# Kernel optimization log

Hardware: AMD Instinct MI355X
Metric: run time of the kernel (lower is better)

Reference implementation:

```python
import jax, jax.numpy as jnp
import numpy as np


def _binarize_except_outliers(weight):
    # torch.mean / torch.std over the flattened weight; torch.std is unbiased (ddof=1)
    mean = jnp.mean(weight)
    std = jnp.std(weight, ddof=1)
    lower = mean - std
    upper = mean + std
    outliers = (weight < lower) | (weight > upper)
    # non-outliers -> sign(w) (STEBinary forward); outliers keep original fp values
    return jnp.where(outliers, weight, jnp.sign(weight))


def setup_inputs() -> dict:
    key = jax.random.key(0)
    k1, k2, k3 = jax.random.split(key, 3)
    B, S, D_IN, D_OUT = 8, 2048, 4096, 4096
    x = jax.random.normal(k1, (B, S, D_IN), dtype=jnp.float32)
    weight = jax.random.normal(k2, (D_OUT, D_IN), dtype=jnp.float32) * 0.02
    bias = jax.random.normal(k3, (D_OUT,), dtype=jnp.float32) * 0.02
    return {"x": x, "weight": weight, "bias": bias}


def reference(x, weight, bias):
    w_bin = _binarize_except_outliers(weight)  # [d_out, d_in]
    # F.linear: x @ w.T + b
    out = jnp.einsum("bsd,od->bso", x, w_bin) + bias
    return out
```

## Files before the change

### kernel.cpp

```cpp
#include <hip/hip_runtime.h>
#include <stdint.h>
#include <math.h>

typedef __attribute__((ext_vector_type(8))) short short8;
typedef __attribute__((ext_vector_type(4))) float f32x4;

typedef const __attribute__((address_space(1))) void* gas_ptr;
typedef __attribute__((address_space(3))) void* las_ptr;

__device__ __forceinline__ void gld_lds16(const void* g, void* l) {
    __builtin_amdgcn_global_load_lds((gas_ptr)g, (las_ptr)l, 16, 0, 0);
}

__device__ __forceinline__ unsigned short f32_to_bf16_rne(float f) {
    unsigned u = __builtin_bit_cast(unsigned, f);
    u += 0x7FFFu + ((u >> 16) & 1u);
    return (unsigned short)(u >> 16);
}

__global__ void stats_partial_kernel(const float* __restrict__ w, int n4, double* __restrict__ partials) {
    __shared__ double ssum[256];
    __shared__ double ssq[256];
    int t = threadIdx.x;
    long i = (long)blockIdx.x * blockDim.x + t;
    long stride = (long)gridDim.x * blockDim.x;
    double s = 0.0, q = 0.0;
    for (; i < n4; i += stride) {
        float4 v = ((const float4*)w)[i];
        s += (double)v.x + (double)v.y + (double)v.z + (double)v.w;
        q += (double)v.x * v.x + (double)v.y * v.y + (double)v.z * v.z + (double)v.w * v.w;
    }
    ssum[t] = s; ssq[t] = q;
    __syncthreads();
    for (int off = 128; off > 0; off >>= 1) {
        if (t < off) { ssum[t] += ssum[t + off]; ssq[t] += ssq[t + off]; }
        __syncthreads();
    }
    if (t == 0) {
        partials[2 * blockIdx.x]     = ssum[0];
        partials[2 * blockIdx.x + 1] = ssq[0];
    }
}

__global__ void stats_final_kernel(const double* __restrict__ partials, int nblocks, long n,
                                   float* __restrict__ bounds) {
    __shared__ double ssum[256];
    __shared__ double ssq[256];
    int t = threadIdx.x;
    double s = 0.0, q = 0.0;
    for (int i = t; i < nblocks; i += 256) {
        s += partials[2 * i];
        q += partials[2 * i + 1];
    }
    ssum[t] = s; ssq[t] = q;
    __syncthreads();
    for (int off = 128; off > 0; off >>= 1) {
        if (t < off) { ssum[t] += ssum[t + off]; ssq[t] += ssq[t + off]; }
        __syncthreads();
    }
    if (t == 0) {
        double sum = ssum[0], sumsq = ssq[0];
        double mean = sum / (double)n;
        double var = (sumsq - sum * sum / (double)n) / (double)(n - 1);
        double sd = sqrt(var);
        bounds[0] = (float)(mean - sd);
        bounds[1] = (float)(mean + sd);
    }
}

__global__ void binarize_w_kernel(const float* __restrict__ w, const float* __restrict__ bounds,
                                  unsigned short* __restrict__ wb, long n4) {
    float lo = bounds[0], hi = bounds[1];
    long i = (long)blockIdx.x * blockDim.x + threadIdx.x;
    if (i >= n4) return;
    float4 v = ((const float4*)w)[i];
    float r[4] = {v.x, v.y, v.z, v.w};
    ushort4 o;
    unsigned short ob[4];
#pragma unroll
    for (int j = 0; j < 4; j++) {
        float f = r[j];
        bool outlier = (f < lo) || (f > hi);
        float b = outlier ? f : (f > 0.f ? 1.f : (f < 0.f ? -1.f : 0.f));
        ob[j] = f32_to_bf16_rne(b);
    }
    o.x = ob[0]; o.y = ob[1]; o.z = ob[2]; o.w = ob[3];
    ((ushort4*)wb)[i] = o;
}

__global__ void convert_x_kernel(const float* __restrict__ x, unsigned short* __restrict__ xb, long n4) {
    long i = (long)blockIdx.x * blockDim.x + threadIdx.x;
    if (i >= n4) return;
    float4 v = ((const float4*)x)[i];
    ushort4 o;
    o.x = f32_to_bf16_rne(v.x);
    o.y = f32_to_bf16_rne(v.y);
    o.z = f32_to_bf16_rne(v.z);
    o.w = f32_to_bf16_rne(v.w);
    ((ushort4*)xb)[i] = o;
}

#define BM 128
#define BN 128
#define BK 64

__global__ __launch_bounds__(256) void gemm_bt_kernel(
    const unsigned short* __restrict__ A,
    const unsigned short* __restrict__ B,
    const float* __restrict__ bias,
    float* __restrict__ C,
    int M, int N, int K)
{
    __shared__ __align__(16) unsigned short As[BM * BK];
    __shared__ __align__(16) unsigned short Bs[BN * BK];

    const int t = threadIdx.x;
    const int wave = t >> 6;
    const int lane = t & 63;
    const int wr = wave >> 1;
    const int wc = wave & 1;
    const int lm = lane & 15;
    const int quad = lane >> 4;
    const int sw = lm & 7;

    const int tile_m = blockIdx.y * BM;
    const int tile_n = blockIdx.x * BN;

    f32x4 acc[4][4] = {};

    int row_[4], src_[4];
#pragma unroll
    for (int j = 0; j < 4; j++) {
        int c = j * 256 + t;
        int r = c >> 3, kc = c & 7;
        row_[j] = r;
        src_[j] = (kc ^ (r & 7)) * 8;
    }
    const int lds_base = wave * 512;

    const size_t Astripe = (size_t)tile_m * K;
    const size_t Bstripe = (size_t)tile_n * K;

    for (int kt = 0; kt < K; kt += BK) {
#pragma unroll
        for (int j = 0; j < 4; j++) {
            gld_lds16(A + Astripe + (size_t)row_[j] * K + kt + src_[j], &As[j * 2048 + lds_base]);
            gld_lds16(B + Bstripe + (size_t)row_[j] * K + kt + src_[j], &Bs[j * 2048 + lds_base]);
        }
        __syncthreads();

#pragma unroll
        for (int s = 0; s < 2; s++) {
            short8 af[4], bf[4];
#pragma unroll
            for (int i = 0; i < 4; i++) {
                int arow = wr * 64 + i * 16 + lm;
                int achunk = (s * 4 + quad) ^ sw;
                af[i] = *(const short8*)&As[arow * 64 + achunk * 8];
                int brow = wc * 64 + i * 16 + lm;
                bf[i] = *(const short8*)&Bs[brow * 64 + achunk * 8];
            }
#pragma unroll
            for (int i = 0; i < 4; i++)
#pragma unroll
                for (int j = 0; j < 4; j++)
                    acc[i][j] = __builtin_amdgcn_mfma_f32_16x16x32_bf16(af[i], bf[j], acc[i][j], 0, 0, 0);
        }
        __syncthreads();
    }

#pragma unroll
    for (int j = 0; j < 4; j++) {
        int col = tile_n + wc * 64 + j * 16 + lm;
        float bv = bias[col];
#pragma unroll
        for (int i = 0; i < 4; i++) {
            int row0 = tile_m + wr * 64 + i * 16 + quad * 4;
#pragma unroll
            for (int r = 0; r < 4; r++) {
                C[(size_t)(row0 + r) * N + col] = acc[i][j][r] + bv;
            }
        }
    }
}

__global__ void gemm_fallback_kernel(const float* __restrict__ A, const float* __restrict__ W,
                                     const float* __restrict__ bias, const float* __restrict__ bounds,
                                     float* __restrict__ C, int M, int N, int K) {
    __shared__ float as[16][16];
    __shared__ float wsm[16][17];
    int tx = threadIdx.x, ty = threadIdx.y;
    int row = blockIdx.y * 16 + ty;
    int col = blockIdx.x * 16 + tx;
    float lo = bounds[0], hi = bounds[1];
    float acc = 0.f;
    for (int k0 = 0; k0 < K; k0 += 16) {
        as[ty][tx] = A[(size_t)row * K + k0 + tx];
        float wv = W[(size_t)(blockIdx.x * 16 + ty) * K + k0 + tx];
        bool outlier = (wv < lo) || (wv > hi);
        wsm[ty][tx] = outlier ? wv : (wv > 0.f ? 1.f : (wv < 0.f ? -1.f : 0.f));
        __syncthreads();
#pragma unroll
        for (int k = 0; k < 16; k++) acc += as[ty][k] * wsm[tx][k];
        __syncthreads();
    }
    C[(size_t)row * N + col] = acc + bias[col];
}

extern "C" void kernel_launch(void* const* d_in, const int* in_sizes, int n_in,
                              void* d_out, int out_size, void* d_ws, size_t ws_size,
                              hipStream_t stream) {
    const float* x    = (const float*)d_in[0];
    const float* w    = (const float*)d_in[1];
    const float* bias = (const float*)d_in[2];
    float* out = (float*)d_out;

    const int  N  = in_sizes[2];
    const long wn = (long)in_sizes[1];
    const int  K  = (int)(wn / N);
    const long xn = (long)in_sizes[0];
    const int  M  = (int)(xn / K);

    char* ws = (char*)d_ws;
    float*  bounds   = (float*)ws;
    double* partials = (double*)(ws + 64);
    const size_t wb_off = 16512;
    unsigned short* wb = (unsigned short*)(ws + wb_off);
    const size_t xb_off = wb_off + (size_t)wn * 2;
    unsigned short* xb = (unsigned short*)(ws + xb_off);
    const size_t need_full = xb_off + (size_t)xn * 2;

    stats_partial_kernel<<<1024, 256, 0, stream>>>(w, (int)(wn / 4), partials);
    stats_final_kernel<<<1, 256, 0, stream>>>(partials, 1024, wn, bounds);

    if (ws_size >= need_full) {
        long wn4 = wn / 4, xn4 = xn / 4;
        binarize_w_kernel<<<(int)((wn4 + 255) / 256), 256, 0, stream>>>(w, bounds, wb, wn4);
        convert_x_kernel<<<(int)((xn4 + 255) / 256), 256, 0, stream>>>(x, xb, xn4);
        dim3 grid(N / BN, M / BM);
        gemm_bt_kernel<<<grid, 256, 0, stream>>>(xb, wb, bias, out, M, N, K);
    } else {
        dim3 grid(N / 16, M / 16), blk(16, 16);
        gemm_fallback_kernel<<<grid, blk, 0, stream>>>(x, w, bias, bounds, out, M, N, K);
    }
}
```

Baseline: 1.206 ms.

## Replace GEMM with 256x256 double-buffered 8-wave pipelined kernel

Replaces the 128x128 single-buffered bf16 MFMA GEMM with a 256x256 tile, 512-thread kernel. It double-buffers LDS and issues global-to-LDS loads in phases interleaved with MFMA work, using explicit waitcnt, barriers and setprio. It also remaps workgroup IDs for L2 locality and vectorizes the convert/binarize kernels into 8-element grid-stride loops. The aim is to hide memory latency and raise arithmetic intensity, at the cost of more LDS (128KB) and registers, which limits occupancy.

```diff
diff --git a/kernel.cpp b/kernel.cpp
--- a/kernel.cpp
+++ b/kernel.cpp
@@ -69,117 +69,166 @@
 }
 
 __global__ void binarize_w_kernel(const float* __restrict__ w, const float* __restrict__ bounds,
-                                  unsigned short* __restrict__ wb, long n4) {
+                                  unsigned short* __restrict__ wb, long n8) {
     float lo = bounds[0], hi = bounds[1];
     long i = (long)blockIdx.x * blockDim.x + threadIdx.x;
-    if (i >= n4) return;
-    float4 v = ((const float4*)w)[i];
-    float r[4] = {v.x, v.y, v.z, v.w};
-    ushort4 o;
-    unsigned short ob[4];
-#pragma unroll
-    for (int j = 0; j < 4; j++) {
-        float f = r[j];
-        bool outlier = (f < lo) || (f > hi);
-        float b = outlier ? f : (f > 0.f ? 1.f : (f < 0.f ? -1.f : 0.f));
-        ob[j] = f32_to_bf16_rne(b);
-    }
-    o.x = ob[0]; o.y = ob[1]; o.z = ob[2]; o.w = ob[3];
-    ((ushort4*)wb)[i] = o;
-}
-
-__global__ void convert_x_kernel(const float* __restrict__ x, unsigned short* __restrict__ xb, long n4) {
+    long stride = (long)gridDim.x * blockDim.x;
+    for (; i < n8; i += stride) {
+        float4 v0 = ((const float4*)w)[2 * i];
+        float4 v1 = ((const float4*)w)[2 * i + 1];
+        float r[8] = {v0.x, v0.y, v0.z, v0.w, v1.x, v1.y, v1.z, v1.w};
+        short8 o;
+#pragma unroll
+        for (int j = 0; j < 8; j++) {
+            float f = r[j];
+            bool outlier = (f < lo) || (f > hi);
+            float b = outlier ? f : (f > 0.f ? 1.f : (f < 0.f ? -1.f : 0.f));
+            o[j] = (short)f32_to_bf16_rne(b);
+        }
+        ((short8*)wb)[i] = o;
+    }
+}
+
+__global__ void convert_x_kernel(const float* __restrict__ x, unsigned short* __restrict__ xb, long n8) {
     long i = (long)blockIdx.x * blockDim.x + threadIdx.x;
-    if (i >= n4) return;
-    float4 v = ((const float4*)x)[i];
-    ushort4 o;
-    o.x = f32_to_bf16_rne(v.x);
-    o.y = f32_to_bf16_rne(v.y);
-    o.z = f32_to_bf16_rne(v.z);
-    o.w = f32_to_bf16_rne(v.w);
-    ((ushort4*)xb)[i] = o;
-}
-
-#define BM 128
-#define BN 128
+    long stride = (long)gridDim.x * blockDim.x;
+    for (; i < n8; i += stride) {
+        float4 v0 = ((const float4*)x)[2 * i];
+        float4 v1 = ((const float4*)x)[2 * i + 1];
+        short8 o;
+        o[0] = (short)f32_to_bf16_rne(v0.x);
+        o[1] = (short)f32_to_bf16_rne(v0.y);
+        o[2] = (short)f32_to_bf16_rne(v0.z);
+        o[3] = (short)f32_to_bf16_rne(v0.w);
+        o[4] = (short)f32_to_bf16_rne(v1.x);
+        o[5] = (short)f32_to_bf16_rne(v1.y);
+        o[6] = (short)f32_to_bf16_rne(v1.z);
+        o[7] = (short)f32_to_bf16_rne(v1.w);
+        ((short8*)xb)[i] = o;
+    }
+}
+
+#define BM 256
+#define BN 256
 #define BK 64
 
-__global__ __launch_bounds__(256) void gemm_bt_kernel(
+__global__ __launch_bounds__(512, 2) void gemm_8phase_kernel(
     const unsigned short* __restrict__ A,
     const unsigned short* __restrict__ B,
     const float* __restrict__ bias,
     float* __restrict__ C,
     int M, int N, int K)
 {
-    __shared__ __align__(16) unsigned short As[BM * BK];
-    __shared__ __align__(16) unsigned short Bs[BN * BK];
+    __shared__ __align__(16) unsigned short As[2][BM * BK];
+    __shared__ __align__(16) unsigned short Bs[2][BN * BK];
 
     const int t = threadIdx.x;
     const int wave = t >> 6;
     const int lane = t & 63;
-    const int wr = wave >> 1;
-    const int wc = wave & 1;
+    const int wm = wave >> 2;
+    const int wn = wave & 3;
     const int lm = lane & 15;
     const int quad = lane >> 4;
-    const int sw = lm & 7;
-
-    const int tile_m = blockIdx.y * BM;
-    const int tile_n = blockIdx.x * BN;
-
-    f32x4 acc[4][4] = {};
-
-    int row_[4], src_[4];
-#pragma unroll
-    for (int j = 0; j < 4; j++) {
-        int c = j * 256 + t;
-        int r = c >> 3, kc = c & 7;
-        row_[j] = r;
-        src_[j] = (kc ^ (r & 7)) * 8;
-    }
-    const int lds_base = wave * 512;
-
-    const size_t Astripe = (size_t)tile_m * K;
-    const size_t Bstripe = (size_t)tile_n * K;
-
-    for (int kt = 0; kt < K; kt += BK) {
-#pragma unroll
-        for (int j = 0; j < 4; j++) {
-            gld_lds16(A + Astripe + (size_t)row_[j] * K + kt + src_[j], &As[j * 2048 + lds_base]);
-            gld_lds16(B + Bstripe + (size_t)row_[j] * K + kt + src_[j], &Bs[j * 2048 + lds_base]);
+
+    const int nwg = gridDim.x;
+    int id = blockIdx.x;
+    if ((nwg & 7) == 0) id = (id & 7) * (nwg >> 3) + (id >> 3);
+    const int nbn = N / BN;
+    const int tile_m = (id / nbn) * BM;
+    const int tile_n = (id % nbn) * BN;
+
+    const int srow = t >> 3;
+    const int scol = ((t & 7) ^ (srow & 7)) * 8;
+    const int lds_wbase = wave * 512;
+
+    const unsigned short* Abase = A + (size_t)tile_m * K;
+    const unsigned short* Bbase = B + (size_t)tile_n * K;
+
+    auto stageA = [&](int u2, int h) {
+        const unsigned short* g = Abase + (size_t)(h * 128 + srow) * K + u2 * BK + scol;
+        unsigned short* l = &As[u2 & 1][h * 8192 + lds_wbase];
+        gld_lds16(g, l);
+        gld_lds16(g + (size_t)64 * K, l + 4096);
+    };
+    auto stageB = [&](int u2, int h) {
+        const unsigned short* g = Bbase + (size_t)(h * 128 + srow) * K + u2 * BK + scol;
+        unsigned short* l = &Bs[u2 & 1][h * 8192 + lds_wbase];
+        gld_lds16(g, l);
+        gld_lds16(g + (size_t)64 * K, l + 4096);
+    };
+
+    stageB(0, 0); stageB(0, 1); stageA(0, 0); stageA(0, 1);
+    stageB(1, 0); stageB(1, 1); stageA(1, 0);
+    asm volatile("s_waitcnt vmcnt(6)" ::: "memory");
+    __builtin_amdgcn_s_barrier();
+
+    f32x4 acc[8][4] = {};
+    short8 bf[4][2];
+
+    const int NT = K / BK;
+    for (int u = 0; u < NT; ++u) {
+        const unsigned short* as = &As[u & 1][0];
+        const unsigned short* bs = &Bs[u & 1][0];
+        const bool s1 = (u + 1 < NT);
+        const bool s2 = (u + 2 < NT);
+
+#pragma unroll
+        for (int q = 0; q < 4; ++q) {
+            if (q == 0)      { if (s1) stageA(u + 1, 1); }
+            else if (q == 1) { if (s2) stageB(u + 2, 0); }
+            else if (q == 2) { if (s2) stageB(u + 2, 1); }
+            else             { if (s2) stageA(u + 2, 0); }
+
+            if (q == 0) {
+#pragma unroll
+                for (int j = 0; j < 4; ++j) {
+                    int brow = wn * 64 + j * 16 + lm;
+#pragma unroll
+                    for (int ks = 0; ks < 2; ++ks)
+                        bf[j][ks] = *(const short8*)&bs[brow * 64 + (((ks * 4 + quad) ^ (brow & 7)) * 8)];
+                }
+            }
+            short8 af[2][2];
+            const int arow0 = q * 64 + wm * 32 + lm;
+#pragma unroll
+            for (int i = 0; i < 2; ++i) {
+                int arow = arow0 + i * 16;
+#pragma unroll
+                for (int ks = 0; ks < 2; ++ks)
+                    af[i][ks] = *(const short8*)&as[arow * 64 + (((ks * 4 + quad) ^ (arow & 7)) * 8)];
+            }
+
+            __builtin_amdgcn_s_barrier();
+            asm volatile("s_waitcnt lgkmcnt(0)" ::: "memory");
+            __builtin_amdgcn_s_setprio(1);
+#pragma unroll
+            for (int ks = 0; ks < 2; ++ks)
+#pragma unroll
+                for (int i = 0; i < 2; ++i)
+#pragma unroll
+                    for (int j = 0; j < 4; ++j)
+                        acc[q * 2 + i][j] = __builtin_amdgcn_mfma_f32_16x16x32_bf16(
+                            af[i][ks], bf[j][ks], acc[q * 2 + i][j], 0, 0, 0);
+            __builtin_amdgcn_s_setprio(0);
+
+            if (q == 3) {
+                if (s2)      { asm volatile("s_waitcnt vmcnt(6)" ::: "memory"); }
+                else if (s1) { asm volatile("s_waitcnt vmcnt(0)" ::: "memory"); }
+            }
+            __builtin_amdgcn_s_barrier();
         }
-        __syncthreads();
-
-#pragma unroll
-        for (int s = 0; s < 2; s++) {
-            short8 af[4], bf[4];
-#pragma unroll
-            for (int i = 0; i < 4; i++) {
-                int arow = wr * 64 + i * 16 + lm;
-                int achunk = (s * 4 + quad) ^ sw;
-                af[i] = *(const short8*)&As[arow * 64 + achunk * 8];
-                int brow = wc * 64 + i * 16 + lm;
-                bf[i] = *(const short8*)&Bs[brow * 64 + achunk * 8];
-            }
-#pragma unroll
-            for (int i = 0; i < 4; i++)
-#pragma unroll
-                for (int j = 0; j < 4; j++)
-                    acc[i][j] = __builtin_amdgcn_mfma_f32_16x16x32_bf16(af[i], bf[j], acc[i][j], 0, 0, 0);
-        }
-        __syncthreads();
-    }
-
-#pragma unroll
-    for (int j = 0; j < 4; j++) {
-        int col = tile_n + wc * 64 + j * 16 + lm;
-        float bv = bias[col];
-#pragma unroll
-        for (int i = 0; i < 4; i++) {
-            int row0 = tile_m + wr * 64 + i * 16 + quad * 4;
-#pragma unroll
-            for (int r = 0; r < 4; r++) {
-                C[(size_t)(row0 + r) * N + col] = acc[i][j][r] + bv;
-            }
+    }
+
+#pragma unroll
+    for (int j = 0; j < 4; ++j) {
+        const int col = tile_n + wn * 64 + j * 16 + lm;
+        const float bv = bias[col];
+#pragma unroll
+        for (int m = 0; m < 8; ++m) {
+            const int row0 = tile_m + (m >> 1) * 64 + wm * 32 + (m & 1) * 16 + quad * 4;
+#pragma unroll
+            for (int r = 0; r < 4; ++r)
+                C[(size_t)(row0 + r) * N + col] = acc[m][j][r] + bv;
         }
     }
 }
@@ -233,12 +282,17 @@
     stats_partial_kernel<<<1024, 256, 0, stream>>>(w, (int)(wn / 4), partials);
     stats_final_kernel<<<1, 256, 0, stream>>>(partials, 1024, wn, bounds);
 
-    if (ws_size >= need_full) {
-        long wn4 = wn / 4, xn4 = xn / 4;
-        binarize_w_kernel<<<(int)((wn4 + 255) / 256), 256, 0, stream>>>(w, bounds, wb, wn4);
-        convert_x_kernel<<<(int)((xn4 + 255) / 256), 256, 0, stream>>>(x, xb, xn4);
-        dim3 grid(N / BN, M / BM);
-        gemm_bt_kernel<<<grid, 256, 0, stream>>>(xb, wb, bias, out, M, N, K);
+    const bool ok256 = (M % 256 == 0) && (N % 256 == 0) && (K % 64 == 0) && (K / 64 >= 3)
+                       && (wn % 8 == 0) && (xn % 8 == 0);
+
+    if (ws_size >= need_full && ok256) {
+        long wn8 = wn / 8, xn8 = xn / 8;
+        int bb = (int)((wn8 + 255) / 256); if (bb > 2048) bb = 2048;
+        int cb = (int)((xn8 + 255) / 256); if (cb > 2048) cb = 2048;
+        binarize_w_kernel<<<bb, 256, 0, stream>>>(w, bounds, wb, wn8);
+        convert_x_kernel<<<cb, 256, 0, stream>>>(x, xb, xn8);
+        dim3 grid((M / BM) * (N / BN));
+        gemm_8phase_kernel<<<grid, 512, 0, stream>>>(xb, wb, bias, out, M, N, K);
     } else {
         dim3 grid(N / 16, M / 16), blk(16, 16);
         gemm_fallback_kernel<<<grid, blk, 0, stream>>>(x, w, bias, bounds, out, M, N, K);
```

Result: faster. 1.083 ms (-10.2%).
